# Performance work log

Hardware: AMD Instinct MI355X
Metric: run time of the kernel (lower is better)

## Reference

```python
import jax, jax.numpy as jnp
import numpy as np

B, C_IN, D_IN, H_IN, W_IN = 2, 96, 16, 64, 64
C = 192
HEADS = 8
DH = C // HEADS
NE = 256
TOPK = 32
DEPTH = 2
STRIDE = (2, 2, 2)
EPS = 1e-5
NEG = -1e9


def setup_inputs() -> dict:
    key = jax.random.key(0)
    ks = jax.random.split(key, 8)
    s = 0.02
    return {
        "x": jax.random.normal(ks[0], (B, C_IN, D_IN, H_IN, W_IN), jnp.float32),
        "conv_w": jax.random.normal(ks[1], (C, C_IN) + STRIDE, jnp.float32) * s,
        "conv_b": jnp.zeros((C,), jnp.float32),
        "bn_gamma": jnp.ones((C,), jnp.float32),
        "bn_beta": jnp.zeros((C,), jnp.float32),
        "bn_mean": jnp.zeros((C,), jnp.float32),
        "bn_var": jnp.ones((C,), jnp.float32),
        "ln_g": jnp.ones((DEPTH, 3, C), jnp.float32),
        "ln_b": jnp.zeros((DEPTH, 3, C), jnp.float32),
        "attn_w": jax.random.normal(ks[2], (DEPTH, 2, 4, C, C), jnp.float32) * s,  # [q,k,v,o]
        "attn_b": jnp.zeros((DEPTH, 2, 4, C), jnp.float32),
        "mlp_w1": jax.random.normal(ks[3], (DEPTH, C, 4 * C), jnp.float32) * s,
        "mlp_b1": jnp.zeros((DEPTH, 4 * C), jnp.float32),
        "mlp_w2": jax.random.normal(ks[4], (DEPTH, 4 * C, C), jnp.float32) * s,
        "mlp_b2": jnp.zeros((DEPTH, C), jnp.float32),
    }


def _ln(x, g, b):
    m = jnp.mean(x, axis=-1, keepdims=True)
    v = jnp.mean(jnp.square(x - m), axis=-1, keepdims=True)
    return (x - m) * jax.lax.rsqrt(v + EPS) * g + b


def _mha(q_in, k_in, v_in, mask, w, b):
    # masked bipartite multi-head attention; mask: (B, Q, Kv) in {0,1}
    Bq, Q, _ = q_in.shape
    Kv = k_in.shape[1]
    q = (q_in @ w[0] + b[0]).reshape(Bq, Q, HEADS, DH)
    k = (k_in @ w[1] + b[1]).reshape(Bq, Kv, HEADS, DH)
    v = (v_in @ w[2] + b[2]).reshape(Bq, Kv, HEADS, DH)
    scores = jnp.einsum('bqhd,bkhd->bhqk', q, k) / jnp.sqrt(jnp.float32(DH))
    scores = jnp.where(mask[:, None, :, :] > 0, scores, NEG)
    attn = jax.nn.softmax(scores, axis=-1)
    out = jnp.einsum('bhqk,bkhd->bqhd', attn, v).reshape(Bq, Q, C)
    out = out @ w[3] + b[3]
    valid = jnp.sum(mask, axis=-1) > 0  # queries with no incident members output 0
    return jnp.where(valid[..., None], out, 0.0)


def _build_hypergraph(x_flat, Dp, Hp, Wp):
    # CS_KNN_3D: evenly-strided center sampling; each hyperedge = K nearest nodes
    # under combined (feature^2 + anisotropic spatial^2) distance, spacing (2,1,1).
    N = Dp * Hp * Wp
    spacing = jnp.array([2.0, 1.0, 1.0], dtype=jnp.float32)
    gd, gh, gw = jnp.meshgrid(jnp.arange(Dp), jnp.arange(Hp), jnp.arange(Wp), indexing='ij')
    coords = jnp.stack([gd, gh, gw], axis=-1).reshape(N, 3).astype(jnp.float32) * spacing
    centers = jnp.round(jnp.linspace(0, N - 1, NE)).astype(jnp.int32)
    cf = x_flat[:, centers, :]                      # (B, Ne, C)
    cp = coords[centers]                            # (Ne, 3)
    feat_d2 = (jnp.sum(cf * cf, -1)[:, :, None] + jnp.sum(x_flat * x_flat, -1)[:, None, :]
               - 2.0 * jnp.einsum('bec,bnc->ben', cf, x_flat))
    spat_d2 = (jnp.sum(cp * cp, -1)[:, None] + jnp.sum(coords * coords, -1)[None, :]
               - 2.0 * cp @ coords.T)               # (Ne, N)
    dist = feat_d2 + spat_d2[None]                  # (B, Ne, N)
    _, idx = jax.lax.top_k(-dist, TOPK)             # (B, Ne, K) nearest nodes per hyperedge
    Bn = x_flat.shape[0]
    Hm = jnp.zeros((Bn, NE, N), jnp.float32).at[
        jnp.arange(Bn)[:, None, None], jnp.arange(NE)[None, :, None], idx].set(1.0)
    return Hm.transpose(0, 2, 1)                    # (B, N, Ne)


def reference(x, conv_w, conv_b, bn_gamma, bn_beta, bn_mean, bn_var,
              ln_g, ln_b, attn_w, attn_b, mlp_w1, mlp_b1, mlp_w2, mlp_b2):
    # downsample: Conv3d(kernel=stride=STRIDE) + BatchNorm3d (eval) + GELU
    y = jax.lax.conv_general_dilated(x, conv_w, window_strides=STRIDE, padding='VALID',
                                     dimension_numbers=('NCDHW', 'OIDHW', 'NCDHW'))
    y = y + conv_b[None, :, None, None, None]
    y = ((y - bn_mean[None, :, None, None, None]) * jax.lax.rsqrt(bn_var + EPS)[None, :, None, None, None]
         * bn_gamma[None, :, None, None, None] + bn_beta[None, :, None, None, None])
    y = jax.nn.gelu(y, approximate=False)
    Bn, Cc, Dp, Hp, Wp = y.shape
    xf = y.reshape(Bn, Cc, Dp * Hp * Wp).transpose(0, 2, 1)  # (B, N, C)
    Hm = _build_hypergraph(xf, Dp, Hp, Wp)                   # (B, N, Ne)
    maskT = Hm.transpose(0, 2, 1)                            # (B, Ne, N)
    deg = jnp.maximum(jnp.sum(Hm, axis=1), 1.0)              # (B, Ne)
    for i in range(DEPTH):
        xn1 = _ln(xf, ln_g[i, 0], ln_b[i, 0])
        he0 = jnp.einsum('bne,bnc->bec', Hm, xn1) / deg[..., None]  # hyperedge init: member mean
        he = _mha(he0, xn1, xn1, maskT, attn_w[i, 0], attn_b[i, 0])  # node -> hyperedge
        xn2 = _ln(xf, ln_g[i, 1], ln_b[i, 1])
        xf = xf + _mha(xn2, he, he, Hm, attn_w[i, 1], attn_b[i, 1])  # hyperedge -> node
        xn3 = _ln(xf, ln_g[i, 2], ln_b[i, 2])
        h = jax.nn.gelu(xn3 @ mlp_w1[i] + mlp_b1[i], approximate=False)
        xf = xf + h @ mlp_w2[i] + mlp_b2[i]
    return xf.transpose(0, 2, 1).reshape(Bn, Cc, Dp, Hp, Wp)
```

## Files before the change

kernel.cpp:

```cpp
#include <hip/hip_runtime.h>
#include <hip/hip_bf16.h>
#include <math.h>

typedef __hip_bfloat16 bf16;
typedef __attribute__((ext_vector_type(8))) short short8v;
typedef __attribute__((ext_vector_type(4))) float float4v;

#define B_ 2
#define CIN 96
#define C_ 192
#define N_ 8192
#define NE_ 256
#define TOPK_ 32
#define HEADS_ 8
#define DH_ 24
#define FF_ 768

__device__ __forceinline__ float b2f(bf16 v) { return __bfloat162float(v); }
__device__ __forceinline__ bf16 f2b(float v) { return __float2bfloat16(v); }
__device__ __forceinline__ unsigned short bfb(float v) {
    union { bf16 b; unsigned short u; } t; t.b = __float2bfloat16(v); return t.u;
}
__device__ __forceinline__ float ldx(const float* p, size_t i) { return p[i]; }
__device__ __forceinline__ float ldx(const bf16* p, size_t i) { return __bfloat162float(p[i]); }
__device__ __forceinline__ void stx(float* p, size_t i, float v) { p[i] = v; }
__device__ __forceinline__ void stx(bf16* p, size_t i, float v) { p[i] = __float2bfloat16(v); }
__device__ __forceinline__ float gelu_f(float x) {
    return 0.5f * x * (1.0f + erff(x * 0.7071067811865475f));
}

__global__ __launch_bounds__(256) void conv_mfma(
    const float* __restrict__ x, const float* __restrict__ cw, const float* __restrict__ cb,
    const float* __restrict__ g, const float* __restrict__ be, const float* __restrict__ mu,
    const float* __restrict__ var, float* __restrict__ xf)
{
    __shared__ unsigned short As[64][40];
    __shared__ unsigned short Bst[64][40];
    int bm = blockIdx.x * 64, bn = blockIdx.y * 64;
    int tid = threadIdx.x;
    int wave = tid >> 6, lane = tid & 63;
    int lrow = lane & 15, lk8 = lane >> 4;
    int r = tid >> 2, kb = (tid & 3) * 8;
    int ng = bm + r;
    int b = ng >> 13, n = ng & 8191;
    int d = n >> 10, h = (n >> 5) & 31, w = n & 31;
    size_t sbase = ((size_t)b * CIN * 16 + 2 * d) * 4096 + (2 * h) * 64 + 2 * w;
    const float* wrow = cw + (size_t)(bn + r) * 768;
    float4v acc[4];
#pragma unroll
    for (int f = 0; f < 4; ++f) acc[f] = (float4v){0.f, 0.f, 0.f, 0.f};
    for (int k0 = 0; k0 < 768; k0 += 32) {
        {
            int ci = (k0 + kb) >> 3;
            const float* xb = x + sbase + (size_t)ci * 16 * 4096;
            float2 t0 = *(const float2*)(xb);
            float2 t1 = *(const float2*)(xb + 64);
            float2 t2 = *(const float2*)(xb + 4096);
            float2 t3 = *(const float2*)(xb + 4160);
            As[r][kb + 0] = bfb(t0.x); As[r][kb + 1] = bfb(t0.y);
            As[r][kb + 2] = bfb(t1.x); As[r][kb + 3] = bfb(t1.y);
            As[r][kb + 4] = bfb(t2.x); As[r][kb + 5] = bfb(t2.y);
            As[r][kb + 6] = bfb(t3.x); As[r][kb + 7] = bfb(t3.y);
        }
        {
            const float* wq = wrow + k0 + kb;
#pragma unroll
            for (int j = 0; j < 8; ++j) Bst[r][kb + j] = bfb(wq[j]);
        }
        __syncthreads();
        short8v av = *(const short8v*)&As[wave * 16 + lrow][lk8 * 8];
#pragma unroll
        for (int f = 0; f < 4; ++f) {
            short8v bv = *(const short8v*)&Bst[f * 16 + lrow][lk8 * 8];
            acc[f] = __builtin_amdgcn_mfma_f32_16x16x32_bf16(av, bv, acc[f], 0, 0, 0);
        }
        __syncthreads();
    }
#pragma unroll
    for (int f = 0; f < 4; ++f) {
        int co = bn + f * 16 + lrow;
        float bias = cb[co];
        float scale = g[co] / sqrtf(var[co] + 1e-5f);
        float mean = mu[co];
        float shift = be[co];
#pragma unroll
        for (int rr = 0; rr < 4; ++rr) {
            int m = bm + wave * 16 + lk8 * 4 + rr;
            float v = (acc[f][rr] + bias - mean) * scale + shift;
            xf[(size_t)m * C_ + co] = gelu_f(v);
        }
    }
}

__global__ __launch_bounds__(256) void row_ss(const float* __restrict__ xf, float* __restrict__ ssb)
{
    int row = blockIdx.x * 4 + (threadIdx.x >> 6);
    int lane = threadIdx.x & 63;
    const float* xr = xf + (size_t)row * C_;
    float x0 = xr[lane], x1 = xr[lane + 64], x2 = xr[lane + 128];
    float s = x0 * x0 + x1 * x1 + x2 * x2;
    for (int off = 32; off; off >>= 1) s += __shfl_xor(s, off, 64);
    if (lane == 0) ssb[row] = s;
}

__global__ __launch_bounds__(256) void dist_gemm(
    const float* __restrict__ xf, const float* __restrict__ ssb, float* __restrict__ D, int b)
{
    __shared__ float As[16][65];
    __shared__ float Bs[16][64];
    __shared__ int ceb[64];
    int bm = blockIdx.x * 64, bn = blockIdx.y * 64;
    int tid = threadIdx.x;
    int tx = tid & 15, ty = tid >> 4;
    if (tid < 64) ceb[tid] = (int)rintf((float)(bm + tid) * (8191.0f / 255.0f));
    __syncthreads();
    float acc[4][4] = {};
    for (int k0 = 0; k0 < C_; k0 += 16) {
        for (int i = tid; i < 1024; i += 256) {
            int m = i >> 4, kk = i & 15;
            As[kk][m] = xf[(size_t)(b * N_ + ceb[m]) * C_ + k0 + kk];
        }
        for (int i = tid; i < 1024; i += 256) {
            int kk = i & 15, n = i >> 4;
            Bs[kk][n] = xf[(size_t)(b * N_ + bn + n) * C_ + k0 + kk];
        }
        __syncthreads();
        for (int kk = 0; kk < 16; ++kk) {
            float av[4], bvv[4];
#pragma unroll
            for (int i = 0; i < 4; ++i) av[i] = As[kk][ty * 4 + i];
#pragma unroll
            for (int j = 0; j < 4; ++j) bvv[j] = Bs[kk][tx * 4 + j];
#pragma unroll
            for (int i = 0; i < 4; ++i)
#pragma unroll
                for (int j = 0; j < 4; ++j) acc[i][j] += av[i] * bvv[j];
        }
        __syncthreads();
    }
#pragma unroll
    for (int i = 0; i < 4; ++i) {
        int m = bm + ty * 4 + i;
        int ce = ceb[ty * 4 + i];
        int dc = ce >> 10, rc = ce & 1023, hc = rc >> 5, wc = rc & 31;
        float cfs = ssb[b * N_ + ce];
#pragma unroll
        for (int j = 0; j < 4; ++j) {
            int n = bn + tx * 4 + j;
            int dn = n >> 10, rn = n & 1023, hn = rn >> 5, wn = rn & 31;
            float fd = 2.0f * (float)(dc - dn), fh = (float)(hc - hn), fw = (float)(wc - wn);
            float dist = cfs + ssb[b * N_ + n] - 2.0f * acc[i][j] + (fd * fd + fh * fh + fw * fw);
            D[(size_t)m * N_ + n] = dist;
        }
    }
}

__global__ __launch_bounds__(256) void topk_select(
    const float* __restrict__ D, int* __restrict__ members,
    unsigned long long* __restrict__ nodemask, int b)
{
    __shared__ float dist[N_];
    __shared__ float wv_[4];
    __shared__ int wi_[4];
    __shared__ int winner;
    int e = blockIdx.x;
    int tid = threadIdx.x;
    int wave = tid >> 6, lane = tid & 63;
    const float* row = D + (size_t)e * N_;
    float lmin = 3.4e38f; int lidx = 0x7fffffff;
    for (int i = 0; i < 32; ++i) {
        int n = tid + (i << 8);
        float v = row[n];
        dist[n] = v;
        if (v < lmin) { lmin = v; lidx = n; }
    }
    for (int k = 0; k < TOPK_; ++k) {
        float v = lmin; int ix = lidx;
#pragma unroll
        for (int off = 32; off; off >>= 1) {
            float ov = __shfl_xor(v, off, 64); int oi = __shfl_xor(ix, off, 64);
            if (ov < v || (ov == v && oi < ix)) { v = ov; ix = oi; }
        }
        if (lane == 0) { wv_[wave] = v; wi_[wave] = ix; }
        __syncthreads();
        if (tid == 0) {
            float bv2 = wv_[0]; int bi2 = wi_[0];
#pragma unroll
            for (int wq = 1; wq < 4; ++wq) {
                float ov = wv_[wq]; int oi = wi_[wq];
                if (ov < bv2 || (ov == bv2 && oi < bi2)) { bv2 = ov; bi2 = oi; }
            }
            winner = bi2;
            int wn = ((unsigned)bi2 < N_) ? bi2 : 0;
            members[(b * NE_ + e) * TOPK_ + k] = wn;
            atomicOr(&nodemask[(size_t)(b * N_ + wn) * 4 + (e >> 6)], 1ull << (e & 63));
        }
        __syncthreads();
        int ix2 = winner;
        if ((ix2 & 255) == tid) {
            dist[ix2] = 3.4e38f;
            lmin = 3.4e38f; lidx = 0x7fffffff;
            for (int i = 0; i < 32; ++i) {
                int n = tid + (i << 8);
                float dv = dist[n];
                if (dv < lmin) { lmin = dv; lidx = n; }
            }
        }
    }
}

__global__ __launch_bounds__(256) void ln_stats(const float* __restrict__ xf, float2* __restrict__ stats)
{
    int row = blockIdx.x * 4 + (threadIdx.x >> 6);
    int lane = threadIdx.x & 63;
    const float* xr = xf + (size_t)row * C_;
    float x0 = xr[lane], x1 = xr[lane + 64], x2 = xr[lane + 128];
    float s = x0 + x1 + x2;
    for (int off = 32; off; off >>= 1) s += __shfl_xor(s, off, 64);
    float m = s * (1.0f / 192.0f);
    float d0 = x0 - m, d1 = x1 - m, d2 = x2 - m;
    float s2 = d0 * d0 + d1 * d1 + d2 * d2;
    for (int off = 32; off; off >>= 1) s2 += __shfl_xor(s2, off, 64);
    float inv = 1.0f / sqrtf(s2 * (1.0f / 192.0f) + 1e-5f);
    if (lane == 0) stats[row] = make_float2(m, inv);
}

__global__ __launch_bounds__(256) void gemm_kv(
    const float* __restrict__ A, const float* __restrict__ wk, const float* __restrict__ wv,
    const float* __restrict__ bk, const float* __restrict__ bvv2,
    float* __restrict__ ke, float* __restrict__ ve, int M)
{
    __shared__ float As[16][65];
    __shared__ float Bs[16][64];
    int bm = blockIdx.x * 64;
    int gn = blockIdx.y * 64;
    int sel = gn >= C_;
    const float* Bw = sel ? wv : wk;
    const float* bias = sel ? bvv2 : bk;
    float* Cc = sel ? ve : ke;
    int bn = sel ? gn - C_ : gn;
    int tid = threadIdx.x;
    int tx = tid & 15, ty = tid >> 4;
    float acc[4][4] = {};
    for (int k0 = 0; k0 < C_; k0 += 16) {
        for (int i = tid; i < 1024; i += 256) {
            int m = i >> 4, kk = i & 15;
            As[kk][m] = A[(size_t)(bm + m) * C_ + k0 + kk];
        }
        for (int i = tid; i < 1024; i += 256) {
            int kk = i >> 6, n = i & 63;
            Bs[kk][n] = Bw[(size_t)(k0 + kk) * C_ + bn + n];
        }
        __syncthreads();
        for (int kk = 0; kk < 16; ++kk) {
            float av[4], bvv[4];
#pragma unroll
            for (int i = 0; i < 4; ++i) av[i] = As[kk][ty * 4 + i];
#pragma unroll
            for (int j = 0; j < 4; ++j) bvv[j] = Bs[kk][tx * 4 + j];
#pragma unroll
            for (int i = 0; i < 4; ++i)
#pragma unroll
                for (int j = 0; j < 4; ++j) acc[i][j] += av[i] * bvv[j];
        }
        __syncthreads();
    }
#pragma unroll
    for (int i = 0; i < 4; ++i) {
#pragma unroll
        for (int j = 0; j < 4; ++j) {
            int m = bm + ty * 4 + i, n = bn + tx * 4 + j;
            Cc[(size_t)m * C_ + n] = acc[i][j] + bias[n];
        }
    }
}

template <int LN, int ACT_GELU, int RESID, typename AT, typename CT>
__global__ __launch_bounds__(256) void gemm_mfma(
    const AT* __restrict__ A, const float2* __restrict__ stats,
    const float* __restrict__ lg, const float* __restrict__ lb,
    const float* __restrict__ Bw, const float* __restrict__ bias,
    CT* __restrict__ Cc, int M, int Nn, int K)
{
    __shared__ unsigned short As[64][40];
    __shared__ unsigned short Bst[64][40];
    int bm = blockIdx.x * 64, bn = blockIdx.y * 64;
    int tid = threadIdx.x;
    int wave = tid >> 6, lane = tid & 63;
    int lrow = lane & 15, lk8 = lane >> 4;
    float4v acc[4];
#pragma unroll
    for (int f = 0; f < 4; ++f) acc[f] = (float4v){0.f, 0.f, 0.f, 0.f};
    for (int k0 = 0; k0 < K; k0 += 32) {
        {
            int r = tid >> 2, kb = (tid & 3) * 8;
            float2 st = LN ? stats[bm + r] : make_float2(0.f, 0.f);
            const AT* arow = A + (size_t)(bm + r) * K + k0 + kb;
#pragma unroll
            for (int j = 0; j < 8; ++j) {
                float a = ldx(arow, j);
                if (LN) a = (a - st.x) * st.y * lg[k0 + kb + j] + lb[k0 + kb + j];
                As[r][kb + j] = bfb(a);
            }
        }
        {
            int k = tid >> 3, nb = (tid & 7) * 8;
            const float* brow = Bw + (size_t)(k0 + k) * Nn + bn + nb;
#pragma unroll
            for (int j = 0; j < 8; ++j) Bst[nb + j][k] = bfb(brow[j]);
        }
        __syncthreads();
        short8v av = *(const short8v*)&As[wave * 16 + lrow][lk8 * 8];
#pragma unroll
        for (int f = 0; f < 4; ++f) {
            short8v bv = *(const short8v*)&Bst[f * 16 + lrow][lk8 * 8];
            acc[f] = __builtin_amdgcn_mfma_f32_16x16x32_bf16(av, bv, acc[f], 0, 0, 0);
        }
        __syncthreads();
    }
#pragma unroll
    for (int f = 0; f < 4; ++f) {
#pragma unroll
        for (int r = 0; r < 4; ++r) {
            int m = bm + wave * 16 + lk8 * 4 + r;
            int n = bn + f * 16 + lrow;
            float v = acc[f][r] + bias[n];
            if (ACT_GELU) v = gelu_f(v);
            size_t idx = (size_t)m * Nn + n;
            if (RESID) v += ldx(Cc, idx);
            stx(Cc, idx, v);
        }
    }
}

__global__ __launch_bounds__(256) void mha1_fused(
    const float* __restrict__ xf, const float2* __restrict__ stats,
    const float* __restrict__ lg, const float* __restrict__ lb,
    const int* __restrict__ members, const bf16* __restrict__ kproj,
    const float* __restrict__ w, const float* __restrict__ bias,
    float* __restrict__ he)
{
    __shared__ int mem[TOPK_];
    __shared__ float2 sst[TOPK_];
    __shared__ float xrows[TOPK_][C_];
    __shared__ float kv[TOPK_][C_];
    __shared__ float h0[C_], q[C_], probs[256], wrow[HEADS_ * C_], ar[C_];
    int b = blockIdx.x >> 8, e = blockIdx.x & 255;
    int tid = threadIdx.x;
    if (tid < TOPK_) {
        int mn = members[(b * NE_ + e) * TOPK_ + tid];
        if ((unsigned)mn >= N_) mn = 0;
        mem[tid] = mn;
        sst[tid] = stats[b * N_ + mn];
    }
    __syncthreads();
    for (int i = tid; i < TOPK_ * C_; i += 256) {
        int j = i / C_, c = i - j * C_;
        float v = xf[(size_t)(b * N_ + mem[j]) * C_ + c];
        xrows[j][c] = (v - sst[j].x) * sst[j].y * lg[c] + lb[c];
        kv[j][c] = b2f(kproj[(size_t)(b * N_ + mem[j]) * C_ + c]);
    }
    __syncthreads();
    if (tid < C_) {
        float s = 0.f;
        for (int j = 0; j < TOPK_; ++j) s += xrows[j][tid];
        h0[tid] = s * (1.0f / 32.0f);
    }
    __syncthreads();
    if (tid < C_) {
        float acc = bias[tid];
        for (int k = 0; k < C_; ++k) acc += h0[k] * w[k * C_ + tid];
        q[tid] = acc;
    }
    __syncthreads();
    {
        int hh = tid >> 5, j = tid & 31;
        float s = 0.f;
        for (int d = 0; d < DH_; ++d) s += q[hh * DH_ + d] * kv[j][hh * DH_ + d];
        s *= 0.20412414523193154f;
        float mx = s;
        for (int off = 16; off; off >>= 1) mx = fmaxf(mx, __shfl_xor(mx, off, 32));
        float ex = expf(s - mx);
        float sm = ex;
        for (int off = 16; off; off >>= 1) sm += __shfl_xor(sm, off, 32);
        probs[tid] = ex / sm;
    }
    __syncthreads();
    for (int i = tid; i < HEADS_ * C_; i += 256) {
        int hh = i / C_, k = i - hh * C_;
        const float* pb = probs + hh * 32;
        float acc = 0.f;
        for (int j = 0; j < TOPK_; ++j) acc += pb[j] * xrows[j][k];
        wrow[i] = acc;
    }
    __syncthreads();
    if (tid < C_) {
        int hh = tid / DH_;
        const float* wv2 = w + 2 * C_ * C_;
        const float* wr2 = wrow + hh * C_;
        float acc = bias[2 * C_ + tid];
        for (int k = 0; k < C_; ++k) acc += wr2[k] * wv2[k * C_ + tid];
        ar[tid] = acc;
    }
    __syncthreads();
    if (tid < C_) {
        const float* wo = w + 3 * C_ * C_;
        float acc = bias[3 * C_ + tid];
        for (int k = 0; k < C_; ++k) acc += ar[k] * wo[k * C_ + tid];
        he[(size_t)(b * NE_ + e) * C_ + tid] = acc;
    }
}

__global__ __launch_bounds__(64) void mha2_attn(
    bf16* __restrict__ sbuf, const float* __restrict__ ke, const float* __restrict__ ve,
    const unsigned long long* __restrict__ nodemask)
{
    __shared__ unsigned short lst[NE_];
    __shared__ int cnt;
    __shared__ float qr[C_], sc[HEADS_ * NE_], hsum[HEADS_];
    int blk = blockIdx.x;
    int b = blk >> 13, n = blk & 8191;
    int tid = threadIdx.x;
    size_t row = (size_t)(b * N_ + n) * C_;
    if (tid == 0) {
        int c = 0;
        for (int wd = 0; wd < 4; ++wd) {
            unsigned long long m = nodemask[(size_t)(b * N_ + n) * 4 + wd];
            while (m) {
                int t = __builtin_ctzll(m);
                lst[c++] = (unsigned short)(wd * 64 + t);
                m &= m - 1;
            }
        }
        cnt = c;
    }
    for (int c = tid; c < C_; c += 64) qr[c] = b2f(sbuf[row + c]);
    __syncthreads();
    int m_ = cnt;
    if (m_ == 0) {
        for (int c = tid; c < C_; c += 64) sbuf[row + c] = f2b(0.0f);
        return;
    }
    int hh = tid >> 3, slot = tid & 7;
    float mx = -3.4e38f;
    for (int j = slot; j < m_; j += 8) {
        const float* kr = ke + (size_t)(b * NE_ + lst[j]) * C_ + hh * DH_;
        const float* qh = qr + hh * DH_;
        float s = 0.f;
        for (int d = 0; d < DH_; ++d) s += qh[d] * kr[d];
        s *= 0.20412414523193154f;
        sc[hh * NE_ + j] = s;
        mx = fmaxf(mx, s);
    }
    for (int off = 4; off; off >>= 1) mx = fmaxf(mx, __shfl_xor(mx, off, 8));
    float sum = 0.f;
    for (int j = slot; j < m_; j += 8) {
        float ex = expf(sc[hh * NE_ + j] - mx);
        sc[hh * NE_ + j] = ex;
        sum += ex;
    }
    for (int off = 4; off; off >>= 1) sum += __shfl_xor(sum, off, 8);
    if (slot == 0) hsum[hh] = sum;
    __syncthreads();
    for (int c = tid; c < C_; c += 64) {
        int h2 = c / DH_;
        float acc = 0.f;
        for (int j = 0; j < m_; ++j) acc += sc[h2 * NE_ + j] * ve[(size_t)(b * NE_ + lst[j]) * C_ + c];
        sbuf[row + c] = f2b(acc / hsum[h2]);
    }
}

__global__ __launch_bounds__(256) void write_out_f32(const float* __restrict__ xf, float* __restrict__ out)
{
    __shared__ float t[64 * 193];
    int blk = blockIdx.x;
    int b = blk >> 7, n0 = (blk & 127) * 64;
    for (int i = threadIdx.x; i < 64 * 192; i += 256) {
        int n = i / 192, c = i - (i / 192) * 192;
        t[n * 193 + c] = xf[(size_t)(b * N_ + n0 + n) * C_ + c];
    }
    __syncthreads();
    for (int i = threadIdx.x; i < 64 * 192; i += 256) {
        int c = i >> 6, n = i & 63;
        out[(size_t)(b * C_ + c) * N_ + n0 + n] = t[n * 193 + c];
    }
}

extern "C" void kernel_launch(void* const* d_in, const int* in_sizes, int n_in,
                              void* d_out, int out_size, void* d_ws, size_t ws_size,
                              hipStream_t stream)
{
    const float* x   = (const float*)d_in[0];
    const float* cw  = (const float*)d_in[1];
    const float* cb  = (const float*)d_in[2];
    const float* bg  = (const float*)d_in[3];
    const float* bb  = (const float*)d_in[4];
    const float* bm  = (const float*)d_in[5];
    const float* bv  = (const float*)d_in[6];
    const float* lng = (const float*)d_in[7];
    const float* lnb = (const float*)d_in[8];
    const float* aw  = (const float*)d_in[9];
    const float* ab  = (const float*)d_in[10];
    const float* m1  = (const float*)d_in[11];
    const float* mb1 = (const float*)d_in[12];
    const float* m2  = (const float*)d_in[13];
    const float* mb2 = (const float*)d_in[14];
    float* out = (float*)d_out;

    float* xf = (float*)d_ws;
    char* ob = (char*)d_out;
    float* D = (float*)ob;
    unsigned long long* nodemask = (unsigned long long*)(ob + 8388608);
    int* members = (int*)(ob + 8912896);
    float* ssb   = (float*)(ob + 8978432);
    bf16* sbuf = (bf16*)ob;
    char* ob2 = ob + 6291456;
    float2* stats = (float2*)(ob2 + 524288);
    float* he     = (float*)(ob2 + 720896);
    float* ke     = (float*)(ob2 + 1114112);
    float* ve     = (float*)(ob2 + 1507328);

    hipMemsetAsync(nodemask, 0, (size_t)B_ * N_ * 4 * sizeof(unsigned long long), stream);

    const int MT = B_ * N_;
    {
        dim3 gc(MT / 64, C_ / 64);
        conv_mfma<<<gc, 256, 0, stream>>>(x, cw, cb, bg, bb, bm, bv, xf);
    }
    row_ss<<<MT / 4, 256, 0, stream>>>(xf, ssb);
    for (int b = 0; b < B_; ++b) {
        dim3 gd(4, N_ / 64);
        dist_gemm<<<gd, 256, 0, stream>>>(xf, ssb, D, b);
        topk_select<<<NE_, 256, 0, stream>>>(D, members, nodemask, b);
    }

    for (int i = 0; i < 2; ++i) {
        const float* w0 = aw + (size_t)((i * 2 + 0) * 4) * C_ * C_;
        const float* b0 = ab + (size_t)((i * 2 + 0) * 4) * C_;
        const float* w1 = aw + (size_t)((i * 2 + 1) * 4) * C_ * C_;
        const float* b1 = ab + (size_t)((i * 2 + 1) * 4) * C_;
        const float* g1 = lng + (i * 3 + 0) * C_, *bb1 = lnb + (i * 3 + 0) * C_;
        const float* g2 = lng + (i * 3 + 1) * C_, *bb2 = lnb + (i * 3 + 1) * C_;
        const float* g3 = lng + (i * 3 + 2) * C_, *bb3 = lnb + (i * 3 + 2) * C_;

        ln_stats<<<MT / 4, 256, 0, stream>>>(xf, stats);
        {
            dim3 gk(MT / 64, C_ / 64);
            gemm_mfma<1, 0, 0, float, bf16><<<gk, 256, 0, stream>>>(
                xf, stats, g1, bb1, w0 + 1 * C_ * C_, b0 + 1 * C_, sbuf, MT, C_, C_);
        }
        mha1_fused<<<B_ * NE_, 256, 0, stream>>>(xf, stats, g1, bb1, members, sbuf, w0, b0, he);

        {
            dim3 ge(B_ * NE_ / 64, 6);
            gemm_kv<<<ge, 256, 0, stream>>>(he, w1 + 1 * C_ * C_, w1 + 2 * C_ * C_,
                                            b1 + 1 * C_, b1 + 2 * C_, ke, ve, B_ * NE_);
            dim3 gq(MT / 64, C_ / 64);
            gemm_mfma<1, 0, 0, float, bf16><<<gq, 256, 0, stream>>>(
                xf, stats, g2, bb2, w1 + 0 * C_ * C_, b1 + 0 * C_, sbuf, MT, C_, C_);
        }
        mha2_attn<<<MT, 64, 0, stream>>>(sbuf, ke, ve, nodemask);
        {
            dim3 go(MT / 64, C_ / 64);
            gemm_mfma<0, 0, 1, bf16, float><<<go, 256, 0, stream>>>(
                sbuf, nullptr, nullptr, nullptr, w1 + 3 * C_ * C_, b1 + 3 * C_, xf, MT, C_, C_);
        }

        ln_stats<<<MT / 4, 256, 0, stream>>>(xf, stats);
        for (int ch = 0; ch < 4; ++ch) {
            int off = ch * 4096;
            dim3 g1d(4096 / 64, FF_ / 64);
            gemm_mfma<1, 1, 0, float, bf16><<<g1d, 256, 0, stream>>>(
                xf + (size_t)off * C_, stats + off, g3, bb3,
                m1 + (size_t)i * C_ * FF_, mb1 + i * FF_, sbuf, 4096, FF_, C_);
            dim3 g2d(4096 / 64, C_ / 64);
            gemm_mfma<0, 0, 1, bf16, float><<<g2d, 256, 0, stream>>>(
                sbuf, nullptr, nullptr, nullptr,
                m2 + (size_t)i * FF_ * C_, mb2 + i * C_, xf + (size_t)off * C_, 4096, C_, FF_);
        }
    }
    write_out_f32<<<B_ * N_ / 64, 256, 0, stream>>>(xf, out);
}
```

Before: 701.8 us.

## Prefetch next conv k-tile into registers and XOR-swizzle LDS tiles

The conv implicit-GEMM kernel now loads the next 32-wide k-slice of input and weights into registers while the current slice is consumed by MFMA, hiding global load latency behind compute. LDS tiles switch from padded rows to an XOR-swizzled layout to avoid bank conflicts on the 16-byte fragment reads. This doubles the LDS footprint of the tiles and adds register pressure from the prefetch buffers.

```diff
diff --git a/kernel.cpp b/kernel.cpp
--- a/kernel.cpp
+++ b/kernel.cpp
@@ -34,13 +34,14 @@
     const float* __restrict__ g, const float* __restrict__ be, const float* __restrict__ mu,
     const float* __restrict__ var, float* __restrict__ xf)
 {
-    __shared__ unsigned short As[64][40];
-    __shared__ unsigned short Bst[64][40];
+    __shared__ unsigned short As[64][64];
+    __shared__ unsigned short Bst[64][64];
     int bm = blockIdx.x * 64, bn = blockIdx.y * 64;
     int tid = threadIdx.x;
     int wave = tid >> 6, lane = tid & 63;
     int lrow = lane & 15, lk8 = lane >> 4;
-    int r = tid >> 2, kb = (tid & 3) * 8;
+    int r = tid >> 2, kbi = tid & 3;
+    int wslot = (kbi ^ (r & 7)) * 8;
     int ng = bm + r;
     int b = ng >> 13, n = ng & 8191;
     int d = n >> 10, h = (n >> 5) & 31, w = n & 31;
@@ -49,30 +50,48 @@
     float4v acc[4];
 #pragma unroll
     for (int f = 0; f < 4; ++f) acc[f] = (float4v){0.f, 0.f, 0.f, 0.f};
+
+    float2 t0, t1, t2, t3;
+    float wreg[8];
+    {
+        int ci = (0 + kbi * 8) >> 3;
+        const float* xb = x + sbase + (size_t)ci * 16 * 4096;
+        t0 = *(const float2*)(xb);
+        t1 = *(const float2*)(xb + 64);
+        t2 = *(const float2*)(xb + 4096);
+        t3 = *(const float2*)(xb + 4160);
+        const float* wq = wrow + kbi * 8;
+#pragma unroll
+        for (int j = 0; j < 8; ++j) wreg[j] = wq[j];
+    }
     for (int k0 = 0; k0 < 768; k0 += 32) {
+        As[r][wslot + 0] = bfb(t0.x); As[r][wslot + 1] = bfb(t0.y);
+        As[r][wslot + 2] = bfb(t1.x); As[r][wslot + 3] = bfb(t1.y);
+        As[r][wslot + 4] = bfb(t2.x); As[r][wslot + 5] = bfb(t2.y);
+        As[r][wslot + 6] = bfb(t3.x); As[r][wslot + 7] = bfb(t3.y);
+#pragma unroll
+        for (int j = 0; j < 8; ++j) Bst[r][wslot + j] = bfb(wreg[j]);
+        __syncthreads();
+        if (k0 + 32 < 768) {
+            int ci = (k0 + 32 + kbi * 8) >> 3;
+            const float* xb = x + sbase + (size_t)ci * 16 * 4096;
+            t0 = *(const float2*)(xb);
+            t1 = *(const float2*)(xb + 64);
+            t2 = *(const float2*)(xb + 4096);
+            t3 = *(const float2*)(xb + 4160);
+            const float* wq = wrow + k0 + 32 + kbi * 8;
+#pragma unroll
+            for (int j = 0; j < 8; ++j) wreg[j] = wq[j];
+        }
         {
-            int ci = (k0 + kb) >> 3;
-            const float* xb = x + sbase + (size_t)ci * 16 * 4096;
-            float2 t0 = *(const float2*)(xb);
-            float2 t1 = *(const float2*)(xb + 64);
-            float2 t2 = *(const float2*)(xb + 4096);
-            float2 t3 = *(const float2*)(xb + 4160);
-            As[r][kb + 0] = bfb(t0.x); As[r][kb + 1] = bfb(t0.y);
-            As[r][kb + 2] = bfb(t1.x); As[r][kb + 3] = bfb(t1.y);
-            As[r][kb + 4] = bfb(t2.x); As[r][kb + 5] = bfb(t2.y);
-            As[r][kb + 6] = bfb(t3.x); As[r][kb + 7] = bfb(t3.y);
-        }
-        {
-            const float* wq = wrow + k0 + kb;
-#pragma unroll
-            for (int j = 0; j < 8; ++j) Bst[r][kb + j] = bfb(wq[j]);
-        }
-        __syncthreads();
-        short8v av = *(const short8v*)&As[wave * 16 + lrow][lk8 * 8];
-#pragma unroll
-        for (int f = 0; f < 4; ++f) {
-            short8v bv = *(const short8v*)&Bst[f * 16 + lrow][lk8 * 8];
-            acc[f] = __builtin_amdgcn_mfma_f32_16x16x32_bf16(av, bv, acc[f], 0, 0, 0);
+            int arow = wave * 16 + lrow;
+            short8v av = *(const short8v*)&As[arow][(lk8 ^ (arow & 7)) * 8];
+#pragma unroll
+            for (int f = 0; f < 4; ++f) {
+                int brow = f * 16 + lrow;
+                short8v bv = *(const short8v*)&Bst[brow][(lk8 ^ (brow & 7)) * 8];
+                acc[f] = __builtin_amdgcn_mfma_f32_16x16x32_bf16(av, bv, acc[f], 0, 0, 0);
+            }
         }
         __syncthreads();
     }
```

After: 703.7 us. About the same (+0.3%).
